# Performance work log

Hardware: AMD Instinct MI355X
Metric: run time of the kernel (lower is better)

## Reference

```python
import jax, jax.numpy as jnp
import numpy as np

B, T, D, H = 4, 2048, 1024, 8
HD = D // H  # head_dim = 128


def setup_inputs() -> dict:
    key = jax.random.key(0)
    ks = jax.random.split(key, 10)
    s = 1.0 / np.sqrt(D)
    return {
        "x": jax.random.normal(ks[0], (B, T, D), jnp.float32),
        "y": jax.random.normal(ks[1], (B, T, D), jnp.float32),
        "Wq": jax.random.normal(ks[2], (D, D), jnp.float32) * s,
        "bq": jnp.zeros((D,), jnp.float32),
        "Wk": jax.random.normal(ks[3], (D, D), jnp.float32) * s,
        "bk": jnp.zeros((D,), jnp.float32),
        "Wv": jax.random.normal(ks[4], (D, D), jnp.float32) * s,
        "bv": jnp.zeros((D,), jnp.float32),
        "Wo": jax.random.normal(ks[5], (D, D), jnp.float32) * s,
        "bo": jnp.zeros((D,), jnp.float32),
    }


def _heads(t):
    # [B, T, D] -> [B, H, T, HD]
    b, t_, _ = t.shape
    return t.reshape(b, t_, H, HD).transpose(0, 2, 1, 3)


def reference(x, y, Wq, bq, Wk, bk, Wv, bv, Wo, bo):
    Tq, Tk = x.shape[1], y.shape[1]
    q = _heads(x @ Wq.T + bq)  # [B,H,Tq,HD]
    k = _heads(y @ Wk.T + bk)  # [B,H,Tk,HD]
    v = _heads(y @ Wv.T + bv)  # [B,H,Tk,HD]
    scale = 1.0 / np.sqrt(HD)
    logits = jnp.einsum("bhqd,bhkd->bhqk", q, k) * scale
    # causal mask: positions k > q get -inf
    causal = jnp.triu(jnp.full((Tq, Tk), -jnp.inf, jnp.float32), k=1)
    logits = logits + causal
    attn = jax.nn.softmax(logits, axis=-1)  # [B,H,Tq,Tk]
    ctx = jnp.einsum("bhqk,bhkd->bhqd", attn, v)
    ctx = ctx.transpose(0, 2, 1, 3).reshape(x.shape[0], Tq, D)
    out = ctx @ Wo.T + bo
    return out
```

## Files before the change

### kernel.cpp

```cpp
#include <hip/hip_runtime.h>
#include <math.h>

#define TB 4
#define TT 2048
#define TD 1024
#define TH 8
#define THD 128

typedef __attribute__((ext_vector_type(8))) short short8;
typedef __attribute__((ext_vector_type(4))) short short4v;
typedef __attribute__((ext_vector_type(4))) float float4v;
typedef __attribute__((ext_vector_type(16))) float float16v;

__device__ __forceinline__ short f2bf(float f) {
    union { float f; unsigned u; } v; v.f = f;
    unsigned r = v.u + 0x7FFFu + ((v.u >> 16) & 1u);
    return (short)(r >> 16);
}

__device__ __forceinline__ short8 cvt8(float4v a, float4v b) {
    short8 r;
    r[0] = f2bf(a[0]); r[1] = f2bf(a[1]); r[2] = f2bf(a[2]); r[3] = f2bf(a[3]);
    r[4] = f2bf(b[0]); r[5] = f2bf(b[1]); r[6] = f2bf(b[2]); r[7] = f2bf(b[3]);
    return r;
}

__device__ __forceinline__ void async16(const void* g, void* l) {
    __builtin_amdgcn_global_load_lds(
        (const __attribute__((address_space(1))) unsigned int*)g,
        (__attribute__((address_space(3))) unsigned int*)l, 16, 0, 0);
}

__global__ void cvtall(const float* __restrict__ x, const float* __restrict__ y,
                       const float* __restrict__ wq, const float* __restrict__ wk,
                       const float* __restrict__ wv, const float* __restrict__ wo,
                       short* __restrict__ xyb, short* __restrict__ wb)
{
    const size_t SZ = (size_t)TB * TT * TD;
    const size_t WSZ = (size_t)TD * TD;
    int ty = blockIdx.y;
    const float* s; short* d; size_t n;
    if (ty == 0)      { s = x;  d = xyb;      n = SZ; }
    else if (ty == 1) { s = y;  d = xyb + SZ; n = SZ; }
    else {
        s = (ty == 2) ? wq : (ty == 3) ? wk : (ty == 4) ? wv : wo;
        d = wb + (size_t)(ty - 2) * WSZ; n = WSZ;
    }
    size_t i = ((size_t)blockIdx.x * blockDim.x + threadIdx.x) * 8;
    if (i >= n) return;
    float4v v0 = *(const float4v*)(s + i);
    float4v v1 = *(const float4v*)(s + i + 4);
    *(short8*)(d + i) = cvt8(v0, v1);
}

__global__ __launch_bounds__(256, 2)
void gemm_qkv(const short* __restrict__ xyb, const short* __restrict__ wb,
              const float* __restrict__ bq, const float* __restrict__ bk,
              const float* __restrict__ bv,
              short* __restrict__ qhp, short* __restrict__ khp,
              short* __restrict__ vtp)
{
    __shared__ __attribute__((aligned(16))) short SMEM[16896];
    short* As = SMEM;
    short* Bs = SMEM + 8192;

    const int n0g = blockIdx.x * 128;
    const int mode = n0g >> 10;
    const int n0 = n0g & 1023;
    const int h_ = n0 >> 7;
    const size_t SZ = (size_t)TB * TT * TD;
    const short* A = (mode == 0) ? xyb : (xyb + SZ);
    const short* W = wb + (size_t)mode * TD * TD;
    const float* bias = (mode == 0) ? bq : (mode == 1) ? bk : bv;
    const float scale = (mode == 0)
        ? (0.08838834764831845f * 1.4426950408889634f) : 1.0f;

    const int tid = threadIdx.x;
    const int lane = tid & 63, wv = tid >> 6;
    const int lr = lane & 15, qd = lane >> 4;
    const int sw = lane & 7;
    const int wm = (wv >> 1) * 64, wn = (wv & 1) * 64;
    const int m0 = blockIdx.y * 128;
    const int K = TD;
    const int rsub = lane >> 3;
    const int gj = ((lane & 7) ^ rsub) * 8;

    float4v acc[4][4];
#pragma unroll
    for (int mt = 0; mt < 4; ++mt)
#pragma unroll
        for (int nt = 0; nt < 4; ++nt)
            acc[mt][nt] = float4v{0.f, 0.f, 0.f, 0.f};

    for (int kb = 0; kb < K; kb += 64) {
#pragma unroll
        for (int p = 0; p < 8; ++p) {
            int ch = wv * 8 + p;
            if (ch < 16) {
                int row = ch * 8 + rsub;
                async16(A + (size_t)(m0 + row) * K + kb + gj, As + ch * 512);
            } else {
                int row = (ch - 16) * 8 + rsub;
                async16(W + (size_t)(n0 + row) * K + kb + gj, Bs + (ch - 16) * 512);
            }
        }
        __syncthreads();

#pragma unroll
        for (int ks = 0; ks < 2; ++ks) {
            short8 af[4], bfr[4];
#pragma unroll
            for (int mt = 0; mt < 4; ++mt)
                af[mt] = *(const short8*)&As[(wm + mt * 16 + lr) * 64 +
                                             ((ks * 4 + qd) ^ sw) * 8];
#pragma unroll
            for (int nt = 0; nt < 4; ++nt)
                bfr[nt] = *(const short8*)&Bs[(wn + nt * 16 + lr) * 64 +
                                              ((ks * 4 + qd) ^ sw) * 8];
#pragma unroll
            for (int mt = 0; mt < 4; ++mt)
#pragma unroll
                for (int nt = 0; nt < 4; ++nt)
                    acc[mt][nt] = __builtin_amdgcn_mfma_f32_16x16x32_bf16(
                        af[mt], bfr[nt], acc[mt][nt], 0, 0, 0);
        }
        __syncthreads();
    }

#pragma unroll
    for (int nt = 0; nt < 4; ++nt) {
        int col = wn + nt * 16 + lr;
        float bi = bias[n0 + col];
#pragma unroll
        for (int mt = 0; mt < 4; ++mt)
#pragma unroll
            for (int i = 0; i < 4; ++i) {
                int row = wm + mt * 16 + qd * 4 + i;
                short v = f2bf((acc[mt][nt][i] + bi) * scale);
                if (mode < 2) SMEM[row * 128 + col] = v;
                else          SMEM[col * 132 + row] = v;
            }
    }
    __syncthreads();

    if (mode < 2) {
        short* outp = (mode == 0) ? qhp : khp;
#pragma unroll
        for (int r8 = 0; r8 < 8; ++r8) {
            int row = r8 * 16 + (tid >> 4), c = tid & 15;
            short8 v = *(const short8*)&SMEM[row * 128 + c * 8];
            int tg = m0 + row;
            int b_ = tg >> 11, t_ = tg & (TT - 1);
            *(short8*)&outp[(((size_t)(b_ * TH + h_)) * TT + t_) * THD + c * 8] = v;
        }
    } else {
        int b_ = m0 >> 11, t0 = m0 & (TT - 1);
#pragma unroll
        for (int r8 = 0; r8 < 8; ++r8) {
            int hd = r8 * 16 + (tid >> 4), c = tid & 15;
            short8 v = *(const short8*)&SMEM[hd * 132 + c * 8];
            *(short8*)&vtp[(((size_t)(b_ * TH + h_)) * THD + hd) * TT + t0 + c * 8] = v;
        }
    }
}

__global__ __launch_bounds__(256, 2)
void gemm_out(const short* __restrict__ A, const short* __restrict__ W,
              const float* __restrict__ bias, float* __restrict__ outp)
{
    __shared__ __attribute__((aligned(16))) short As[128 * 64];
    __shared__ __attribute__((aligned(16))) short Bs[128 * 64];

    const int tid = threadIdx.x;
    const int lane = tid & 63, wv = tid >> 6;
    const int lr = lane & 15, qd = lane >> 4;
    const int sw = lane & 7;
    const int wm = (wv >> 1) * 64, wn = (wv & 1) * 64;
    const int m0 = blockIdx.y * 128, n0 = blockIdx.x * 128;
    const int K = TD;
    const int rsub = lane >> 3;
    const int gj = ((lane & 7) ^ rsub) * 8;

    float4v acc[4][4];
#pragma unroll
    for (int mt = 0; mt < 4; ++mt)
#pragma unroll
        for (int nt = 0; nt < 4; ++nt)
            acc[mt][nt] = float4v{0.f, 0.f, 0.f, 0.f};

    for (int kb = 0; kb < K; kb += 64) {
#pragma unroll
        for (int p = 0; p < 8; ++p) {
            int ch = wv * 8 + p;
            if (ch < 16) {
                int row = ch * 8 + rsub;
                async16(A + (size_t)(m0 + row) * K + kb + gj, As + ch * 512);
            } else {
                int row = (ch - 16) * 8 + rsub;
                async16(W + (size_t)(n0 + row) * K + kb + gj, Bs + (ch - 16) * 512);
            }
        }
        __syncthreads();

#pragma unroll
        for (int ks = 0; ks < 2; ++ks) {
            short8 af[4], bfr[4];
#pragma unroll
            for (int mt = 0; mt < 4; ++mt)
                af[mt] = *(const short8*)&As[(wm + mt * 16 + lr) * 64 +
                                             ((ks * 4 + qd) ^ sw) * 8];
#pragma unroll
            for (int nt = 0; nt < 4; ++nt)
                bfr[nt] = *(const short8*)&Bs[(wn + nt * 16 + lr) * 64 +
                                              ((ks * 4 + qd) ^ sw) * 8];
#pragma unroll
            for (int mt = 0; mt < 4; ++mt)
#pragma unroll
                for (int nt = 0; nt < 4; ++nt)
                    acc[mt][nt] = __builtin_amdgcn_mfma_f32_16x16x32_bf16(
                        af[mt], bfr[nt], acc[mt][nt], 0, 0, 0);
        }
        __syncthreads();
    }

#pragma unroll
    for (int nt = 0; nt < 4; ++nt) {
        int col = n0 + wn + nt * 16 + lr;
        float bi = bias[col];
#pragma unroll
        for (int mt = 0; mt < 4; ++mt)
#pragma unroll
            for (int i = 0; i < 4; ++i) {
                int row = m0 + wm + mt * 16 + qd * 4 + i;
                outp[(size_t)row * TD + col] = acc[mt][nt][i] + bi;
            }
    }
}

__global__ __launch_bounds__(256, 2)
void attn_fwd(const short* __restrict__ qh, const short* __restrict__ kh,
              const short* __restrict__ vt, short* __restrict__ ctx)
{
    __shared__ __attribute__((aligned(16))) short Ks[64 * 128];
    __shared__ __attribute__((aligned(16))) short Vs[128 * 64];

    const int tid = threadIdx.x;
    const int lane = tid & 63, wv = tid >> 6;
    const int l31 = lane & 31, h = lane >> 5;
    const int sw7 = l31 & 7;

    const int bi = blockIdx.x;
    const int bh = bi & 31;
    const int grp = bi >> 5;
    const int qt = (grp < 8) ? (15 - grp) : (grp - 8);
    const int b_ = bh >> 3, h_ = bh & 7;
    const size_t bho = (size_t)bh * TT * THD;

    short8 qf[8];
    {
        const short* qp = qh + bho + (size_t)(qt * 128 + wv * 32 + l31) * THD;
#pragma unroll
        for (int ks = 0; ks < 8; ++ks)
            qf[ks] = *(const short8*)(qp + ks * 16 + h * 8);
    }
    float16v o[4];
#pragma unroll
    for (int db = 0; db < 4; ++db)
#pragma unroll
        for (int r = 0; r < 16; ++r) o[db][r] = 0.f;
    float li = 0.f;

    const int nkv = 2 * qt + 2;
    for (int kv = 0; kv < nkv; ++kv) {
        __syncthreads();
        {
            const short* kbase = kh + bho + (size_t)kv * 64 * THD;
            const short* vbase = vt + (size_t)bh * THD * TT + (size_t)kv * 64;
#pragma unroll
            for (int p = 0; p < 4; ++p) {
                int ch = wv * 4 + p;
                int krow = ch * 4 + (lane >> 4);
                int kg = (lane & 15) ^ (krow & 7);
                async16(kbase + (size_t)krow * THD + kg * 8, Ks + ch * 512);
                int vrow = ch * 8 + (lane >> 3);
                int vg = (lane & 7) ^ (vrow & 7);
                async16(vbase + (size_t)vrow * TT + vg * 8, Vs + ch * 512);
            }
        }
        __syncthreads();

        float16v s[2];
#pragma unroll
        for (int kb = 0; kb < 2; ++kb)
#pragma unroll
            for (int r = 0; r < 16; ++r) s[kb][r] = 0.f;
#pragma unroll
        for (int ks = 0; ks < 8; ++ks) {
            int cidx = ((ks * 2 + h) ^ sw7) * 8;
            short8 kf0 = *(const short8*)&Ks[l31 * 128 + cidx];
            short8 kf1 = *(const short8*)&Ks[(32 + l31) * 128 + cidx];
            s[0] = __builtin_amdgcn_mfma_f32_32x32x16_bf16(kf0, qf[ks], s[0], 0, 0, 0);
            s[1] = __builtin_amdgcn_mfma_f32_32x32x16_bf16(kf1, qf[ks], s[1], 0, 0, 0);
        }

        if (kv >= 2 * qt) {
            int q = qt * 128 + wv * 32 + l31;
#pragma unroll
            for (int r = 0; r < 16; ++r) {
                int key = kv * 64 + (r & 3) + 8 * (r >> 2) + 4 * h;
                if (key > q) s[0][r] = -1e30f;
                if (key + 32 > q) s[1][r] = -1e30f;
            }
        }

#pragma unroll
        for (int st = 0; st < 8; ++st) {
            float e0 = exp2f(s[st >> 2][(st & 3) * 4 + 0]);
            float e1 = exp2f(s[st >> 2][(st & 3) * 4 + 1]);
            float e2 = exp2f(s[st >> 2][(st & 3) * 4 + 2]);
            float e3 = exp2f(s[st >> 2][(st & 3) * 4 + 3]);
            li += (e0 + e1) + (e2 + e3);
            short4v ap;
            ap[0] = f2bf(e0); ap[1] = f2bf(e1);
            ap[2] = f2bf(e2); ap[3] = f2bf(e3);
#pragma unroll
            for (int db = 0; db < 4; ++db) {
                short4v vf = *(const short4v*)&Vs[(db * 32 + l31) * 64 +
                                                  ((st ^ sw7) * 8) + h * 4];
                o[db] = __builtin_amdgcn_mfma_f32_32x32x8bf16_1k(ap, vf, o[db], 0, 0, 0);
            }
        }
    }

    li += __shfl_xor(li, 32);
    float linv = 1.f / li;
#pragma unroll
    for (int r = 0; r < 16; ++r) {
        int ql = (r & 3) + 8 * (r >> 2) + 4 * h;
        float lv = __shfl(linv, ql, 32);
        int tg = qt * 128 + wv * 32 + ql;
        short* cp = ctx + ((size_t)(b_ * TT + tg)) * TD + h_ * THD + l31;
#pragma unroll
        for (int db = 0; db < 4; ++db)
            cp[db * 32] = f2bf(o[db][r] * lv);
    }
}

extern "C" void kernel_launch(void* const* d_in, const int* in_sizes, int n_in,
                              void* d_out, int out_size, void* d_ws, size_t ws_size,
                              hipStream_t stream) {
    (void)in_sizes; (void)n_in; (void)out_size; (void)ws_size;
    const float* x  = (const float*)d_in[0];
    const float* y  = (const float*)d_in[1];
    const float* Wq = (const float*)d_in[2];
    const float* bq = (const float*)d_in[3];
    const float* Wk = (const float*)d_in[4];
    const float* bk = (const float*)d_in[5];
    const float* Wv = (const float*)d_in[6];
    const float* bv = (const float*)d_in[7];
    const float* Wo = (const float*)d_in[8];
    const float* bo = (const float*)d_in[9];
    float* out = (float*)d_out;

    const size_t SZ = (size_t)TB * TT * TD;
    const size_t WSZ = (size_t)TD * TD;
    short* xyb = (short*)d_ws;
    short* wb  = xyb + 2 * SZ;
    short* qh  = wb + 4 * WSZ;
    short* kh  = qh + SZ;
    short* vt  = kh + SZ;
    short* ctx = xyb;

    dim3 blk(256);

    hipLaunchKernelGGL(cvtall, dim3(SZ / 2048, 6), blk, 0, stream,
                       x, y, Wq, Wk, Wv, Wo, xyb, wb);
    hipLaunchKernelGGL(gemm_qkv, dim3(24, 64), blk, 0, stream,
                       xyb, wb, bq, bk, bv, qh, kh, vt);
    hipLaunchKernelGGL(attn_fwd, dim3(512), blk, 0, stream, qh, kh, vt, ctx);
    hipLaunchKernelGGL(gemm_out, dim3(8, 64), blk, 0, stream,
                       ctx, wb + 3 * WSZ, bo, out);
}
```

Measured before the change: 306.3 us.

## Split causal attention into balanced KV halves with double-buffered K/V and combine kernel

Each attention block now handles two units: query tile j over KV tiles 0..j, and query tile 15-j over its upper KV range. This gives every block the same number of KV tiles instead of letting the longest causal tiles set the runtime. Partial unnormalized outputs (bf16) and row sums go to scratch, and a new combine kernel adds the halves, normalizes and writes ctx. K/V loads are also double-buffered so the next tile is prefetched during compute. The costs are an extra kernel launch, extra scratch traffic, doubled LDS per block, and rounding the partials to bf16.

```diff
diff --git a/kernel.cpp b/kernel.cpp
--- a/kernel.cpp
+++ b/kernel.cpp
@@ -16,6 +16,12 @@
     union { float f; unsigned u; } v; v.f = f;
     unsigned r = v.u + 0x7FFFu + ((v.u >> 16) & 1u);
     return (short)(r >> 16);
+}
+
+__device__ __forceinline__ float bf2f(short s) {
+    union { unsigned u; float f; } v;
+    v.u = ((unsigned)(unsigned short)s) << 16;
+    return v.f;
 }
 
 __device__ __forceinline__ short8 cvt8(float4v a, float4v b) {
@@ -239,111 +245,159 @@
 
 __global__ __launch_bounds__(256, 2)
 void attn_fwd(const short* __restrict__ qh, const short* __restrict__ kh,
-              const short* __restrict__ vt, short* __restrict__ ctx)
+              const short* __restrict__ vt, short* __restrict__ po,
+              float* __restrict__ pl)
 {
-    __shared__ __attribute__((aligned(16))) short Ks[64 * 128];
-    __shared__ __attribute__((aligned(16))) short Vs[128 * 64];
+    __shared__ __attribute__((aligned(16))) short Ks[2][64 * 128];
+    __shared__ __attribute__((aligned(16))) short Vs[2][128 * 64];
 
     const int tid = threadIdx.x;
-    const int lane = tid & 63, wv = tid >> 6;
+    const int lane = tid & 63, wid = tid >> 6;
     const int l31 = lane & 31, h = lane >> 5;
     const int sw7 = l31 & 7;
 
     const int bi = blockIdx.x;
     const int bh = bi & 31;
-    const int grp = bi >> 5;
-    const int qt = (grp < 8) ? (15 - grp) : (grp - 8);
-    const int b_ = bh >> 3, h_ = bh & 7;
+    const int j  = bi >> 5;
     const size_t bho = (size_t)bh * TT * THD;
 
-    short8 qf[8];
-    {
-        const short* qp = qh + bho + (size_t)(qt * 128 + wv * 32 + l31) * THD;
-#pragma unroll
-        for (int ks = 0; ks < 8; ++ks)
-            qf[ks] = *(const short8*)(qp + ks * 16 + h * 8);
-    }
-    float16v o[4];
-#pragma unroll
-    for (int db = 0; db < 4; ++db)
-#pragma unroll
-        for (int r = 0; r < 16; ++r) o[db][r] = 0.f;
-    float li = 0.f;
-
-    const int nkv = 2 * qt + 2;
-    for (int kv = 0; kv < nkv; ++kv) {
+    for (int u = 0; u < 2; ++u) {
+        const int qt  = u ? (15 - j) : j;
+        const int kv0 = u ? (qt + 1) : 0;
+        const int kv1 = u ? (2 * qt + 2) : (j + 1);
+
+        short8 qf[8];
+        {
+            const short* qp = qh + bho + (size_t)(qt * 128 + wid * 32 + l31) * THD;
+#pragma unroll
+            for (int ks = 0; ks < 8; ++ks)
+                qf[ks] = *(const short8*)(qp + ks * 16 + h * 8);
+        }
+        float16v o[4];
+#pragma unroll
+        for (int db = 0; db < 4; ++db)
+#pragma unroll
+            for (int r = 0; r < 16; ++r) o[db][r] = 0.f;
+        float li = 0.f;
+
+        {
+            const short* kbase = kh + bho + (size_t)kv0 * 64 * THD;
+            const short* vbase = vt + (size_t)bh * THD * TT + (size_t)kv0 * 64;
+#pragma unroll
+            for (int p = 0; p < 4; ++p) {
+                int ch = wid * 4 + p;
+                int kr = ch * 4 + (lane >> 4);
+                int kg = (lane & 15) ^ (kr & 7);
+                async16(kbase + (size_t)kr * THD + kg * 8, &Ks[0][ch * 512]);
+                int vr = ch * 8 + (lane >> 3);
+                int vg = (lane & 7) ^ (vr & 7);
+                async16(vbase + (size_t)vr * TT + vg * 8, &Vs[0][ch * 512]);
+            }
+        }
         __syncthreads();
-        {
-            const short* kbase = kh + bho + (size_t)kv * 64 * THD;
-            const short* vbase = vt + (size_t)bh * THD * TT + (size_t)kv * 64;
-#pragma unroll
-            for (int p = 0; p < 4; ++p) {
-                int ch = wv * 4 + p;
-                int krow = ch * 4 + (lane >> 4);
-                int kg = (lane & 15) ^ (krow & 7);
-                async16(kbase + (size_t)krow * THD + kg * 8, Ks + ch * 512);
-                int vrow = ch * 8 + (lane >> 3);
-                int vg = (lane & 7) ^ (vrow & 7);
-                async16(vbase + (size_t)vrow * TT + vg * 8, Vs + ch * 512);
-            }
-        }
-        __syncthreads();
-
-        float16v s[2];
-#pragma unroll
-        for (int kb = 0; kb < 2; ++kb)
-#pragma unroll
-            for (int r = 0; r < 16; ++r) s[kb][r] = 0.f;
-#pragma unroll
-        for (int ks = 0; ks < 8; ++ks) {
-            int cidx = ((ks * 2 + h) ^ sw7) * 8;
-            short8 kf0 = *(const short8*)&Ks[l31 * 128 + cidx];
-            short8 kf1 = *(const short8*)&Ks[(32 + l31) * 128 + cidx];
-            s[0] = __builtin_amdgcn_mfma_f32_32x32x16_bf16(kf0, qf[ks], s[0], 0, 0, 0);
-            s[1] = __builtin_amdgcn_mfma_f32_32x32x16_bf16(kf1, qf[ks], s[1], 0, 0, 0);
-        }
-
-        if (kv >= 2 * qt) {
-            int q = qt * 128 + wv * 32 + l31;
-#pragma unroll
-            for (int r = 0; r < 16; ++r) {
-                int key = kv * 64 + (r & 3) + 8 * (r >> 2) + 4 * h;
-                if (key > q) s[0][r] = -1e30f;
-                if (key + 32 > q) s[1][r] = -1e30f;
-            }
-        }
-
-#pragma unroll
-        for (int st = 0; st < 8; ++st) {
-            float e0 = exp2f(s[st >> 2][(st & 3) * 4 + 0]);
-            float e1 = exp2f(s[st >> 2][(st & 3) * 4 + 1]);
-            float e2 = exp2f(s[st >> 2][(st & 3) * 4 + 2]);
-            float e3 = exp2f(s[st >> 2][(st & 3) * 4 + 3]);
-            li += (e0 + e1) + (e2 + e3);
-            short4v ap;
-            ap[0] = f2bf(e0); ap[1] = f2bf(e1);
-            ap[2] = f2bf(e2); ap[3] = f2bf(e3);
-#pragma unroll
-            for (int db = 0; db < 4; ++db) {
-                short4v vf = *(const short4v*)&Vs[(db * 32 + l31) * 64 +
-                                                  ((st ^ sw7) * 8) + h * 4];
-                o[db] = __builtin_amdgcn_mfma_f32_32x32x8bf16_1k(ap, vf, o[db], 0, 0, 0);
-            }
-        }
-    }
-
-    li += __shfl_xor(li, 32);
-    float linv = 1.f / li;
-#pragma unroll
-    for (int r = 0; r < 16; ++r) {
-        int ql = (r & 3) + 8 * (r >> 2) + 4 * h;
-        float lv = __shfl(linv, ql, 32);
-        int tg = qt * 128 + wv * 32 + ql;
-        short* cp = ctx + ((size_t)(b_ * TT + tg)) * TD + h_ * THD + l31;
-#pragma unroll
-        for (int db = 0; db < 4; ++db)
-            cp[db * 32] = f2bf(o[db][r] * lv);
-    }
+
+        int cur = 0;
+        for (int kv = kv0; kv < kv1; ++kv) {
+            if (kv + 1 < kv1) {
+                const short* kbase = kh + bho + (size_t)(kv + 1) * 64 * THD;
+                const short* vbase = vt + (size_t)bh * THD * TT +
+                                     (size_t)(kv + 1) * 64;
+#pragma unroll
+                for (int p = 0; p < 4; ++p) {
+                    int ch = wid * 4 + p;
+                    int kr = ch * 4 + (lane >> 4);
+                    int kg = (lane & 15) ^ (kr & 7);
+                    async16(kbase + (size_t)kr * THD + kg * 8,
+                            &Ks[cur ^ 1][ch * 512]);
+                    int vr = ch * 8 + (lane >> 3);
+                    int vg = (lane & 7) ^ (vr & 7);
+                    async16(vbase + (size_t)vr * TT + vg * 8,
+                            &Vs[cur ^ 1][ch * 512]);
+                }
+            }
+
+            const short* Kc = Ks[cur];
+            const short* Vc = Vs[cur];
+
+            float16v s[2];
+#pragma unroll
+            for (int kb = 0; kb < 2; ++kb)
+#pragma unroll
+                for (int r = 0; r < 16; ++r) s[kb][r] = 0.f;
+#pragma unroll
+            for (int ks = 0; ks < 8; ++ks) {
+                int cidx = ((ks * 2 + h) ^ sw7) * 8;
+                short8 kf0 = *(const short8*)&Kc[l31 * 128 + cidx];
+                short8 kf1 = *(const short8*)&Kc[(32 + l31) * 128 + cidx];
+                s[0] = __builtin_amdgcn_mfma_f32_32x32x16_bf16(kf0, qf[ks], s[0], 0, 0, 0);
+                s[1] = __builtin_amdgcn_mfma_f32_32x32x16_bf16(kf1, qf[ks], s[1], 0, 0, 0);
+            }
+
+            if (kv >= 2 * qt) {
+                int q = qt * 128 + wid * 32 + l31;
+#pragma unroll
+                for (int r = 0; r < 16; ++r) {
+                    int key = kv * 64 + (r & 3) + 8 * (r >> 2) + 4 * h;
+                    if (key > q) s[0][r] = -1e30f;
+                    if (key + 32 > q) s[1][r] = -1e30f;
+                }
+            }
+
+#pragma unroll
+            for (int st = 0; st < 8; ++st) {
+                float e0 = exp2f(s[st >> 2][(st & 3) * 4 + 0]);
+                float e1 = exp2f(s[st >> 2][(st & 3) * 4 + 1]);
+                float e2 = exp2f(s[st >> 2][(st & 3) * 4 + 2]);
+                float e3 = exp2f(s[st >> 2][(st & 3) * 4 + 3]);
+                li += (e0 + e1) + (e2 + e3);
+                short4v ap;
+                ap[0] = f2bf(e0); ap[1] = f2bf(e1);
+                ap[2] = f2bf(e2); ap[3] = f2bf(e3);
+#pragma unroll
+                for (int db = 0; db < 4; ++db) {
+                    short4v vf = *(const short4v*)&Vc[(db * 32 + l31) * 64 +
+                                                      ((st ^ sw7) * 8) + h * 4];
+                    o[db] = __builtin_amdgcn_mfma_f32_32x32x8bf16_1k(ap, vf, o[db], 0, 0, 0);
+                }
+            }
+            __syncthreads();
+            cur ^= 1;
+        }
+
+        li += __shfl_xor(li, 32);
+        const int slot = (bh * 16 + qt) * 2 + u;
+        if (h == 0) pl[slot * 128 + wid * 32 + l31] = li;
+        short* pop = po + (size_t)slot * 16384 + (size_t)(wid * 32) * 128 + l31;
+#pragma unroll
+        for (int r = 0; r < 16; ++r) {
+            int ql = (r & 3) + 8 * (r >> 2) + 4 * h;
+#pragma unroll
+            for (int db = 0; db < 4; ++db)
+                pop[(size_t)ql * 128 + db * 32] = f2bf(o[db][r]);
+        }
+    }
+}
+
+__global__ __launch_bounds__(256)
+void combine(const short* __restrict__ po, const float* __restrict__ pl,
+             short* __restrict__ ctx)
+{
+    const unsigned i = blockIdx.x * 256 + threadIdx.x;
+    const int hdv = i & 15;
+    const int q   = (i >> 4) & 127;
+    const int qt  = (i >> 11) & 15;
+    const int bh  = i >> 15;
+    const int tile = bh * 16 + qt;
+    const size_t base = (size_t)tile * 2 * 16384 + (size_t)q * 128 + hdv * 8;
+    short8 a = *(const short8*)&po[base];
+    short8 b = *(const short8*)&po[base + 16384];
+    const float inv = 1.f / (pl[tile * 2 * 128 + q] + pl[(tile * 2 + 1) * 128 + q]);
+    short8 r;
+#pragma unroll
+    for (int k = 0; k < 8; ++k)
+        r[k] = f2bf((bf2f(a[k]) + bf2f(b[k])) * inv);
+    const int b_ = bh >> 3, h_ = bh & 7, t = qt * 128 + q;
+    *(short8*)&ctx[((size_t)(b_ * TT + t)) * TD + h_ * THD + hdv * 8] = r;
 }
 
 extern "C" void kernel_launch(void* const* d_in, const int* in_sizes, int n_in,
@@ -369,7 +423,9 @@
     short* qh  = wb + 4 * WSZ;
     short* kh  = qh + SZ;
     short* vt  = kh + SZ;
-    short* ctx = xyb;
+    float* pl  = (float*)(vt + SZ);
+    short* po  = xyb;
+    short* ctx = qh;
 
     dim3 blk(256);
 
@@ -377,7 +433,8 @@
                        x, y, Wq, Wk, Wv, Wo, xyb, wb);
     hipLaunchKernelGGL(gemm_qkv, dim3(24, 64), blk, 0, stream,
                        xyb, wb, bq, bk, bv, qh, kh, vt);
-    hipLaunchKernelGGL(attn_fwd, dim3(512), blk, 0, stream, qh, kh, vt, ctx);
+    hipLaunchKernelGGL(attn_fwd, dim3(512), blk, 0, stream, qh, kh, vt, po, pl);
+    hipLaunchKernelGGL(combine, dim3(4096), blk, 0, stream, po, pl, ctx);
     hipLaunchKernelGGL(gemm_out, dim3(8, 64), blk, 0, stream,
                        ctx, wb + 3 * WSZ, bo, out);
 }
```

Measured after the change: 292.9 us. 1.05x faster.
